# Optimization experiments

Hardware: AMD Instinct MI355X
Metric: run time of the kernel (lower is better)

The kernel has to match this reference:

```python
import jax, jax.numpy as jnp
import numpy as np

B, T, N, D, H = 16, 16, 184, 128, 8
HD = D // H  # 16
EMB = 10


def _forward(dim, query, key, value, Wq, bq, Wk, bk, Wv, bv, Wm, bm, Wo, bo, ne1, ne2):
    B0 = query.shape[0]
    D0 = Wq.shape[0]
    HD0 = Wm.shape[0]
    H0 = D0 // HD0
    q = query @ Wq.T + bq
    k = key @ Wk.T + bk
    v = value @ Wv.T + bv

    def split_heads(x):  # [B, A, C, D] -> [H*B, A, C, HD], head-major (torch split+cat)
        x = x.reshape(x.shape[:-1] + (H0, HD0))
        x = jnp.moveaxis(x, -2, 0)  # [H, B, A, C, HD]
        return x.reshape((H0 * B0,) + x.shape[2:])

    q, k, v = split_heads(q), split_heads(k), split_heads(v)
    # attention over the last spatial axis: scores [H*B, T, N, N]
    attn = jnp.matmul(q, jnp.swapaxes(k, -1, -2)) / jnp.sqrt(jnp.asarray(HD0, q.dtype))
    attn_row = jax.nn.softmax(attn, axis=-1)
    attn_col = jax.nn.softmax(attn, axis=-2)
    o1 = jnp.matmul(attn_row, v)
    o2 = jnp.matmul(jnp.swapaxes(attn_col, -1, -2), v)
    adp = ne1 @ ne2  # [184, 184]
    adp_row = jax.nn.softmax(adp, axis=-1)
    adp_col = jax.nn.softmax(adp, axis=0)
    if dim == 2:
        o3 = jnp.einsum('ik,btkf->btif', adp_row, v)
        o4 = jnp.einsum('ik,btkf->btif', adp_col.T, v)
        out = jnp.concatenate([o1, o2, o3, o4], axis=-1)  # [H*B, T, N, 4*HD]
        out = out @ Wm.T + bm  # [H*B, T, N, HD]
    else:  # dim == 1
        o3 = jnp.einsum('ik,bktf->bitf', adp_row, v)
        o4 = jnp.einsum('ik,bktf->bitf', adp_col.T, v)
        cat = jnp.concatenate([o1, o2, o3, o4], axis=-1)
        filt = cat @ Wm.T + bm
        gate = jnp.tanh(cat[..., :HD0]) * jax.nn.sigmoid(cat[..., -HD0:])
        out = filt + gate
    # merge heads back: [H*B, ..., HD] -> [B, ..., H*HD]
    out = out.reshape((H0, B0) + out.shape[1:])
    out = jnp.moveaxis(out, 0, -2)
    out = out.reshape(out.shape[:-2] + (H0 * HD0,))
    return out @ Wo.T + bo


def setup_inputs() -> dict:
    rng = jax.random.key(0)
    ks = jax.random.split(rng, 16)
    n = lambda i, shape, s=1.0: jax.random.normal(ks[i], shape, dtype=jnp.float32) * s
    return {
        'query': n(0, (B, T, N, D)),
        'key': n(1, (B, T, N, D)),
        'value': n(2, (B, T, N, D)),
        'Wq': n(3, (D, D), 0.05), 'bq': n(4, (D,), 0.05),
        'Wk': n(5, (D, D), 0.05), 'bk': n(6, (D,), 0.05),
        'Wv': n(7, (D, D), 0.05), 'bv': n(8, (D,), 0.05),
        'Wm': n(9, (HD, 4 * HD), 0.05), 'bm': n(10, (HD,), 0.05),
        'Wo': n(11, (D, D), 0.05), 'bo': n(12, (D,), 0.05),
        'ne1': n(13, (N, EMB)),
        'ne2': n(14, (EMB, N)),
        'dim': 2,
    }


def reference(query, key, value, Wq, bq, Wk, bk, Wv, bv, Wm, bm, Wo, bo, ne1, ne2, dim):
    return _forward(dim, query, key, value, Wq, bq, Wk, bk, Wv, bv, Wm, bm, Wo, bo, ne1, ne2)
```

## Files before the change

kernel.cpp:

```cpp
#include <hip/hip_runtime.h>

typedef unsigned int u32;
typedef unsigned short u16;
typedef unsigned long long ull;

constexpr int kB = 16, kT = 16, kN = 184, kD = 128, kH = 8, kHD = 16;
constexpr int kBT = kB * kT;
constexpr int kRows = kBT * kN;
constexpr int kTile = kN * kHD;
#define KQSCALE 0.36067376022224085f

typedef __attribute__((ext_vector_type(8))) short bf16x8;
typedef __attribute__((ext_vector_type(4))) float f32x4;

union FragU {
  bf16x8 f;
  ull u[2];
  uint4 q;
  u16 h[8];
};

#define MFMA(a, b, c) __builtin_amdgcn_mfma_f32_16x16x32_bf16((a), (b), (c), 0, 0, 0)

__device__ __forceinline__ float bf2f(u16 v) {
  return __uint_as_float(((u32)v) << 16);
}
__device__ __forceinline__ u16 f2bf(float f) {
  u32 x = __float_as_uint(f);
  x += 0x7fffu + ((x >> 16) & 1u);
  return (u16)(x >> 16);
}
__device__ __forceinline__ u32 pack_bf2(float lo, float hi) {
  u32 a = __float_as_uint(lo); a += 0x7fffu + ((a >> 16) & 1u);
  u32 b = __float_as_uint(hi); b += 0x7fffu + ((b >> 16) & 1u);
  return __builtin_amdgcn_perm(b, a, 0x07060302);
}
__device__ __forceinline__ u32 pack_trunc(float lo, float hi) {
  return __builtin_amdgcn_perm(__float_as_uint(hi), __float_as_uint(lo), 0x07060302);
}
__device__ __forceinline__ u16 trunc_bf(float f) {
  return (u16)(__float_as_uint(f) >> 16);
}

__global__ __launch_bounds__(256) void proj_kernel(
    const float* __restrict__ qin, const float* __restrict__ kin, const float* __restrict__ vin,
    const float* __restrict__ Wq, const float* __restrict__ Wk, const float* __restrict__ Wv,
    const float* __restrict__ bq, const float* __restrict__ bk, const float* __restrict__ bv,
    u16* __restrict__ qo, u16* __restrict__ ko, u16* __restrict__ vo,
    const float* __restrict__ ne1, const float* __restrict__ ne2,
    u16* __restrict__ arr3, u16* __restrict__ arr4) {
  __shared__ float smem_f[17408];
  const int tid = threadIdx.x;

  if (blockIdx.y == 3) {
    if (blockIdx.x >= 12) return;
    float* const s1  = smem_f;
    float* const s2  = smem_f + 1840;
    float* const l1r = smem_f + 3680;
    float* const l2c = smem_f + 3864;

    for (int i = tid; i < kN * 10; i += 256) { s1[i] = ne1[i]; s2[i] = ne2[i]; }
    __syncthreads();

    if (tid < kN) {
      const int r = tid;
      float reg[10];
#pragma unroll
      for (int e = 0; e < 10; ++e) reg[e] = s1[r * 10 + e];
      float sum = 0.f;
      for (int c = 0; c < kN; ++c) {
        float d = 0.f;
#pragma unroll
        for (int e = 0; e < 10; ++e) d += reg[e] * s2[e * kN + c];
        sum += __expf(d);
      }
      l1r[r] = sum;

      const int c = tid;
      float regc[10];
#pragma unroll
      for (int e = 0; e < 10; ++e) regc[e] = s2[e * kN + c];
      sum = 0.f;
      for (int r2 = 0; r2 < kN; ++r2) {
        float d = 0.f;
#pragma unroll
        for (int e = 0; e < 10; ++e) d += s1[r2 * 10 + e] * regc[e];
        sum += __expf(d);
      }
      l2c[c] = sum;
    }
    __syncthreads();

    for (int ee = blockIdx.x * 256 + tid; ee < 12 * 6 * 64; ee += 12 * 256) {
      const int i = ee / 384;
      const int rem = ee - i * 384;
      const int p = rem >> 6;
      const int lane = rem & 63;
      const int row = i * 16 + (lane & 15);
      const int cb = p * 32 + (lane >> 4) * 8;
      FragU fo3, fo4;
      const bool rok = row < kN;
      float inv1 = 0.f, inv2 = 0.f;
      float rreg[10], creg[10];
      if (rok) {
        inv1 = 1.f / l1r[row];
        inv2 = 1.f / l2c[row];
#pragma unroll
        for (int e = 0; e < 10; ++e) {
          rreg[e] = s1[row * 10 + e];
          creg[e] = s2[e * kN + row];
        }
      }
#pragma unroll
      for (int j = 0; j < 8; ++j) {
        const int col = cb + j;
        float v3 = 0.f, v4 = 0.f;
        if (rok && col < kN) {
          float d3 = 0.f, d4 = 0.f;
#pragma unroll
          for (int e = 0; e < 10; ++e) {
            d3 += rreg[e] * s2[e * kN + col];
            d4 += s1[col * 10 + e] * creg[e];
          }
          v3 = __expf(d3) * inv1;
          v4 = __expf(d4) * inv2;
        }
        fo3.h[j] = f2bf(v3);
        fo4.h[j] = f2bf(v4);
      }
      *(uint4*)(arr3 + (size_t)ee * 8) = fo3.q;
      *(uint4*)(arr4 + (size_t)ee * 8) = fo4.q;
    }
    return;
  }

  u16* const s_w = (u16*)smem_f;
  u16* const s_a = (u16*)smem_f + 128 * 136;

  const float* in; const float* Wf; const float* bias; u16* out; float scale;
  if (blockIdx.y == 0)      { in = qin; Wf = Wq; bias = bq; out = qo; scale = KQSCALE; }
  else if (blockIdx.y == 1) { in = kin; Wf = Wk; bias = bk; out = ko; scale = 1.f; }
  else                      { in = vin; Wf = Wv; bias = bv; out = vo; scale = 1.f; }

  const int r0 = blockIdx.x * 128;
  {
    for (int i = tid; i < 2048; i += 256) {
      const int row = i >> 4, c8 = (i & 15) * 8;
      const float4 w0 = *(const float4*)(Wf + row * 128 + c8);
      const float4 w1 = *(const float4*)(Wf + row * 128 + c8 + 4);
      *(uint4*)(s_w + row * 136 + c8) =
          make_uint4(pack_bf2(w0.x, w0.y), pack_bf2(w0.z, w0.w),
                     pack_bf2(w1.x, w1.y), pack_bf2(w1.z, w1.w));
    }
    const float* abase = in + (size_t)r0 * 128;
#pragma unroll
    for (int i = 0; i < 16; ++i) {
      const int idx = i * 1024 + tid * 4;
      const float4 v = *(const float4*)(abase + idx);
      const int row = idx >> 7, col = idx & 127;
      *(u32*)(s_a + row * 136 + col)     = pack_bf2(v.x, v.y);
      *(u32*)(s_a + row * 136 + col + 2) = pack_bf2(v.z, v.w);
    }
  }
  __syncthreads();

  const int w = tid >> 6, lane = tid & 63, quad = lane >> 4, m = lane & 15;

  f32x4 acc0[8], acc1[8];
  const f32x4 z4 = {0.f, 0.f, 0.f, 0.f};
#pragma unroll
  for (int ct = 0; ct < 8; ++ct) { acc0[ct] = z4; acc1[ct] = z4; }

  const u16* ap0 = s_a + (w * 16 + m) * 136 + quad * 8;
  const u16* ap1 = ap0 + 64 * 136;

#pragma unroll
  for (int kp = 0; kp < 4; ++kp) {
    FragU a0; a0.q = *(const uint4*)(ap0 + kp * 32);
    FragU a1; a1.q = *(const uint4*)(ap1 + kp * 32);
#pragma unroll
    for (int ct = 0; ct < 8; ++ct) {
      FragU bfr; bfr.q = *(const uint4*)(s_w + (ct * 16 + m) * 136 + kp * 32 + quad * 8);
      acc0[ct] = MFMA(a0.f, bfr.f, acc0[ct]);
      acc1[ct] = MFMA(a1.f, bfr.f, acc1[ct]);
    }
  }

  float bc[8];
#pragma unroll
  for (int ct = 0; ct < 8; ++ct) bc[ct] = bias[ct * 16 + m];

#pragma unroll
  for (int half = 0; half < 2; ++half) {
    const f32x4* acc = half ? acc1 : acc0;
    const int rbase = r0 + (w + half * 4) * 16 + quad * 4;
#pragma unroll
    for (int rr = 0; rr < 4; ++rr) {
      const int r = rbase + rr;
      const int bt = r / kN;
      const int n = r - bt * kN;
      u16* op = out + ((size_t)bt * kN + n) * 16 + m;
#pragma unroll
      for (int ct = 0; ct < 8; ++ct)
        op[(size_t)ct * kBT * kN * 16] = f2bf((acc[ct][rr] + bc[ct]) * scale);
    }
  }
}

__global__ __launch_bounds__(256, 2) void attn_kernel(
    const u16* qg, const u16* __restrict__ kg, const u16* __restrict__ vg,
    const u16* __restrict__ arr3, const u16* __restrict__ arr4,
    const float* __restrict__ Wm, const float* __restrict__ bm,
    u16* mg) {
  __shared__ u16 pool[39424];
  u16* const s_E   = pool;
  u16* const s_ET0 = pool + 13824;
  u16* const s_ET1 = pool + 26624;
  u16* const s_vT  = s_ET1;
  u16* const s_cat = s_ET1;

  const int tid = threadIdx.x;
  const size_t base = (size_t)blockIdx.x * kTile;
  const int w = tid >> 6, lane = tid & 63;
  const int quad = lane >> 4, m = lane & 15;

  for (int idx = tid; idx < 3072; idx += 256) {
    const int t = idx >> 4, ch = idx & 15;
    s_vT[ch * 200 + t] = (t < kN) ? vg[base + idx] : (u16)0;
  }

  bf16x8 kfr[12];
#pragma unroll
  for (int t12 = 0; t12 < 12; ++t12) {
    FragU fk; fk.u[0] = 0; fk.u[1] = 0;
    const int tok = t12 * 16 + m;
    if (quad < 2 && tok < kN)
      fk.q = *(const uint4*)(kg + base + tok * 16 + quad * 8);
    kfr[t12] = fk.f;
  }
  bf16x8 qB[3];
#pragma unroll
  for (int ti = 0; ti < 3; ++ti) {
    FragU fq; fq.u[0] = 0; fq.u[1] = 0;
    const int tok = (w + ti * 4) * 16 + m;
    if (quad < 2 && tok < kN)
      fq.q = *(const uint4*)(qg + base + tok * 16 + quad * 8);
    qB[ti] = fq.f;
  }

  bf16x8 wmb[2];
#pragma unroll
  for (int kt = 0; kt < 2; ++kt) {
    FragU f;
#pragma unroll
    for (int j = 0; j < 8; ++j) {
      const int kdl = quad * 8 + j;
      const int orig = (kt * 2 + (kdl & 1)) * 16 + (kdl >> 1);
      f.h[j] = f2bf(Wm[m * 64 + orig]);
    }
    wmb[kt] = f.f;
  }
  const float4 bm4 = *(const float4*)(bm + quad * 4);

  __syncthreads();

  bf16x8 vb[6];
#pragma unroll
  for (int p = 0; p < 6; ++p) {
    FragU f;
    f.q = *(const uint4*)(s_vT + m * 200 + p * 32 + quad * 8);
    vb[p] = f.f;
  }
  FragU onesU; onesU.u[0] = 0x3F803F803F803F80ULL; onesU.u[1] = onesU.u[0];
  const bf16x8 ones = onesU.f;
  const f32x4 zero4 = {0.f, 0.f, 0.f, 0.f};

  f32x4 o1[3], l1[3], o3[3], o4[3], o2[3], l2[3];
#pragma unroll
  for (int ti = 0; ti < 3; ++ti) {
    o1[ti] = zero4; l1[ti] = zero4; o3[ti] = zero4;
    o4[ti] = zero4; o2[ti] = zero4; l2[ti] = zero4;
  }

#define S_PHASE(CC, ETB)                                                      \
  do {                                                                        \
    _Pragma("unroll") for (int ti = 0; ti < 3; ++ti) {                        \
      const int qt = w + ti * 4;                                              \
      const int qrow = qt * 16 + m;                                           \
      _Pragma("unroll") for (int ktl = 0; ktl < 4; ++ktl) {                   \
        f32x4 sv = MFMA(kfr[(CC) * 4 + ktl], qB[ti], zero4);                  \
        const float e0 = exp2f(sv[0]), e1 = exp2f(sv[1]);                     \
        const float e2 = exp2f(sv[2]), e3 = exp2f(sv[3]);                     \
        uint2 ev;                                                             \
        ev.x = pack_trunc(e0, e1);                                            \
        ev.y = pack_trunc(e2, e3);                                            \
        *(uint2*)(s_E + qrow * 72 + ktl * 16 + quad * 4) = ev;                \
        u16* etp = (ETB) + (ktl * 16 + quad * 4) * 200 + qrow;                \
        etp[0]   = trunc_bf(e0);                                              \
        etp[200] = trunc_bf(e1);                                              \
        etp[400] = trunc_bf(e2);                                              \
        etp[600] = trunc_bf(e3);                                              \
      }                                                                       \
    }                                                                         \
  } while (0)

#define LOAD_ARR(CC)                                                          \
  _Pragma("unroll") for (int ti = 0; ti < 3; ++ti) {                          \
    const int qt = w + ti * 4;                                                \
    _Pragma("unroll") for (int pl = 0; pl < 2; ++pl) {                        \
      const int pg = (CC) * 2 + pl;                                           \
      a3f[ti * 2 + pl].q = *(const uint4*)(arr3 + (size_t)((qt * 6 + pg) * 64 + lane) * 8); \
      a4f[ti * 2 + pl].q = *(const uint4*)(arr4 + (size_t)((qt * 6 + pg) * 64 + lane) * 8); \
    }                                                                         \
  }

#define ROW_PHASE(CC)                                                         \
  _Pragma("unroll") for (int ti = 0; ti < 3; ++ti) {                          \
    const int qt = w + ti * 4;                                                \
    const u16* erp = s_E + (qt * 16 + m) * 72 + quad * 8;                     \
    _Pragma("unroll") for (int pl = 0; pl < 2; ++pl) {                        \
      const int pg = (CC) * 2 + pl;                                           \
      FragU pa; pa.q = *(const uint4*)(erp + pl * 32);                        \
      o1[ti] = MFMA(pa.f, vb[pg], o1[ti]);                                    \
      l1[ti] = MFMA(pa.f, ones, l1[ti]);                                      \
      o3[ti] = MFMA(a3f[ti * 2 + pl].f, vb[pg], o3[ti]);                      \
      o4[ti] = MFMA(a4f[ti * 2 + pl].f, vb[pg], o4[ti]);                      \
    }                                                                         \
  }

#define COL_PHASE(CC, ETB)                                                    \
  {                                                                           \
    const u16* etr = (ETB) + (w * 16 + m) * 200 + quad * 8;                   \
    _Pragma("unroll") for (int pg = 0; pg < 6; ++pg) {                        \
      FragU pT; pT.q = *(const uint4*)(etr + pg * 32);                        \
      o2[CC] = MFMA(pT.f, vb[pg], o2[CC]);                                    \
      l2[CC] = MFMA(pT.f, ones, l2[CC]);                                      \
    }                                                                         \
  }

  S_PHASE(0, s_ET0);
  __syncthreads();
  {
    FragU a3f[6], a4f[6];
    LOAD_ARR(0);
    COL_PHASE(0, s_ET0);
    ROW_PHASE(0);
    S_PHASE(1, s_ET1);
  }
  __syncthreads();
  {
    FragU a3f[6], a4f[6];
    LOAD_ARR(1);
    COL_PHASE(1, s_ET1);
    ROW_PHASE(1);
    S_PHASE(2, s_ET0);
  }
  __syncthreads();
  {
    FragU a3f[6], a4f[6];
    LOAD_ARR(2);
    COL_PHASE(2, s_ET0);
    ROW_PHASE(2);
  }

#undef S_PHASE
#undef LOAD_ARR
#undef ROW_PHASE
#undef COL_PHASE

  u16* cw = s_cat + w * 1152;
#pragma unroll
  for (int ti = 0; ti < 3; ++ti) {
    const int tt = w + ti * 4;
#pragma unroll
    for (int r = 0; r < 4; ++r) {
      const int token = quad * 4 + r;
      const float n1 = o1[ti][r] * __builtin_amdgcn_rcpf(l1[ti][r] - 8.0f);
      const float n2 = o2[ti][r] * __builtin_amdgcn_rcpf(l2[ti][r] - 8.0f);
      *(u32*)(cw + token * 72 + 2 * m)      = pack_bf2(n1, n2);
      *(u32*)(cw + token * 72 + 32 + 2 * m) = pack_bf2(o3[ti][r], o4[ti][r]);
    }
    f32x4 macc = {bm4.x, bm4.y, bm4.z, bm4.w};
#pragma unroll
    for (int kt = 0; kt < 2; ++kt) {
      FragU ca; ca.q = *(const uint4*)(cw + m * 72 + kt * 32 + quad * 8);
      macc = MFMA(wmb[kt], ca.f, macc);
    }
    if (tt * 16 + m < kN) {
      *(uint2*)(mg + base + (tt * 16 + m) * 16 + quad * 4) =
          make_uint2(pack_bf2(macc[0], macc[1]), pack_bf2(macc[2], macc[3]));
    }
  }
}

__global__ __launch_bounds__(256) void out_kernel(
    const u16* __restrict__ mg, const float* __restrict__ Wo,
    const float* __restrict__ bo, float* __restrict__ outg) {
  __shared__ u16 s_w[128 * 136];
  const int tid = threadIdx.x;
  {
    for (int i = tid; i < 2048; i += 256) {
      const int row = i >> 4, c8 = (i & 15) * 8;
      const float4 w0 = *(const float4*)(Wo + row * 128 + c8);
      const float4 w1 = *(const float4*)(Wo + row * 128 + c8 + 4);
      *(uint4*)(s_w + row * 136 + c8) =
          make_uint4(pack_bf2(w0.x, w0.y), pack_bf2(w0.z, w0.w),
                     pack_bf2(w1.x, w1.y), pack_bf2(w1.z, w1.w));
    }
  }
  __syncthreads();

  const int w = tid >> 6, lane = tid & 63, quad = lane >> 4, m = lane & 15;
  const int r0 = blockIdx.x * 128;

  f32x4 acc0[8], acc1[8];
  const f32x4 z4 = {0.f, 0.f, 0.f, 0.f};
#pragma unroll
  for (int ct = 0; ct < 8; ++ct) { acc0[ct] = z4; acc1[ct] = z4; }

  const int hh = quad >> 1, hd8 = (quad & 1) * 8;
  const int ra = r0 + w * 16 + m;
  const int bt0 = ra / kN, n0 = ra - bt0 * kN;
  const int rb = ra + 64;
  const int bt1 = rb / kN, n1 = rb - bt1 * kN;
  const u16* mp0 = mg + ((size_t)(hh * kBT + bt0) * kN + n0) * 16 + hd8;
  const u16* mp1 = mg + ((size_t)(hh * kBT + bt1) * kN + n1) * 16 + hd8;
  const size_t hstep = (size_t)2 * kBT * kN * 16;

#pragma unroll
  for (int kp = 0; kp < 4; ++kp) {
    FragU a0; a0.q = *(const uint4*)(mp0 + kp * hstep);
    FragU a1; a1.q = *(const uint4*)(mp1 + kp * hstep);
#pragma unroll
    for (int ct = 0; ct < 8; ++ct) {
      FragU bfr; bfr.q = *(const uint4*)(s_w + (ct * 16 + m) * 136 + kp * 32 + quad * 8);
      acc0[ct] = MFMA(a0.f, bfr.f, acc0[ct]);
      acc1[ct] = MFMA(a1.f, bfr.f, acc1[ct]);
    }
  }

  float bc[8];
#pragma unroll
  for (int ct = 0; ct < 8; ++ct) bc[ct] = bo[ct * 16 + m];

#pragma unroll
  for (int half = 0; half < 2; ++half) {
    const f32x4* acc = half ? acc1 : acc0;
    const int rbase = r0 + (w + half * 4) * 16 + quad * 4;
#pragma unroll
    for (int rr = 0; rr < 4; ++rr) {
      float* op = outg + (size_t)(rbase + rr) * 128 + m;
#pragma unroll
      for (int ct = 0; ct < 8; ++ct)
        op[ct * 16] = acc[ct][rr] + bc[ct];
    }
  }
}

extern "C" void kernel_launch(void* const* d_in, const int* in_sizes, int n_in,
                              void* d_out, int out_size, void* d_ws, size_t ws_size,
                              hipStream_t stream) {
  const float* query = (const float*)d_in[0];
  const float* key   = (const float*)d_in[1];
  const float* value = (const float*)d_in[2];
  const float* Wq = (const float*)d_in[3];
  const float* bq = (const float*)d_in[4];
  const float* Wk = (const float*)d_in[5];
  const float* bk = (const float*)d_in[6];
  const float* Wv = (const float*)d_in[7];
  const float* bv = (const float*)d_in[8];
  const float* Wm = (const float*)d_in[9];
  const float* bm = (const float*)d_in[10];
  const float* Wo = (const float*)d_in[11];
  const float* bo = (const float*)d_in[12];
  const float* ne1 = (const float*)d_in[13];
  const float* ne2 = (const float*)d_in[14];

  const size_t tensor_bytes = (size_t)kH * kB * kT * kN * kHD * 2;
  const size_t frag_bytes = (size_t)12 * 6 * 64 * 8 * 2;
  char* ws = (char*)d_ws;
  u16* qs   = (u16*)(ws);
  u16* ks   = (u16*)(ws + tensor_bytes);
  u16* vs   = (u16*)(ws + 2 * tensor_bytes);
  u16* arr3 = (u16*)(ws + 3 * tensor_bytes);
  u16* arr4 = (u16*)(ws + 3 * tensor_bytes + frag_bytes);

  proj_kernel<<<dim3(kRows / 128, 4), 256, 0, stream>>>(
      query, key, value, Wq, Wk, Wv, bq, bk, bv, qs, ks, vs,
      ne1, ne2, arr3, arr4);
  attn_kernel<<<kH * kB * kT, 256, 0, stream>>>(qs, ks, vs, arr3, arr4, Wm, bm, qs);
  out_kernel<<<kRows / 128, 256, 0, stream>>>(qs, Wo, bo, (float*)d_out);
}
```

Baseline: 230.0 us.

## Fuse QKV projection into attention kernel, split adaptive-adjacency into own kernel

The separate QKV projection kernel is removed. Each attention block now projects its own head's q, k and v slices from the fp32 inputs with MFMA and keeps them in shared memory, so the bf16 q/k/v tensors no longer round-trip through global memory. The adjacency softmax work moves into a small standalone kernel. The cost is that each input row is now read once per head (8 times) instead of once, and each block does extra MFMA work before the attention phase, traded against the saved global writes and reads.

Result: slower. 292.8 us (+27.3%).

```diff
diff --git a/kernel.cpp b/kernel.cpp
--- a/kernel.cpp
+++ b/kernel.cpp
@@ -42,192 +42,183 @@
   return (u16)(__float_as_uint(f) >> 16);
 }
 
-__global__ __launch_bounds__(256) void proj_kernel(
+__global__ __launch_bounds__(256) void adp_kernel(
+    const float* __restrict__ ne1, const float* __restrict__ ne2,
+    u16* __restrict__ arr3, u16* __restrict__ arr4) {
+  __shared__ float s1[kN * 10];
+  __shared__ float s2[10 * kN];
+  __shared__ float l1r[kN];
+  __shared__ float l2c[kN];
+  const int tid = threadIdx.x;
+  for (int i = tid; i < kN * 10; i += 256) { s1[i] = ne1[i]; s2[i] = ne2[i]; }
+  __syncthreads();
+
+  if (tid < kN) {
+    const int r = tid;
+    float reg[10];
+#pragma unroll
+    for (int e = 0; e < 10; ++e) reg[e] = s1[r * 10 + e];
+    float sum = 0.f;
+    for (int c = 0; c < kN; ++c) {
+      float d = 0.f;
+#pragma unroll
+      for (int e = 0; e < 10; ++e) d += reg[e] * s2[e * kN + c];
+      sum += __expf(d);
+    }
+    l1r[r] = sum;
+
+    const int c = tid;
+    float regc[10];
+#pragma unroll
+    for (int e = 0; e < 10; ++e) regc[e] = s2[e * kN + c];
+    sum = 0.f;
+    for (int r2 = 0; r2 < kN; ++r2) {
+      float d = 0.f;
+#pragma unroll
+      for (int e = 0; e < 10; ++e) d += s1[r2 * 10 + e] * regc[e];
+      sum += __expf(d);
+    }
+    l2c[c] = sum;
+  }
+  __syncthreads();
+
+  for (int ee = blockIdx.x * 256 + tid; ee < 12 * 6 * 64; ee += 12 * 256) {
+    const int i = ee / 384;
+    const int rem = ee - i * 384;
+    const int p = rem >> 6;
+    const int lane = rem & 63;
+    const int row = i * 16 + (lane & 15);
+    const int cb = p * 32 + (lane >> 4) * 8;
+    FragU fo3, fo4;
+    const bool rok = row < kN;
+    float inv1 = 0.f, inv2 = 0.f;
+    float rreg[10], creg[10];
+    if (rok) {
+      inv1 = 1.f / l1r[row];
+      inv2 = 1.f / l2c[row];
+#pragma unroll
+      for (int e = 0; e < 10; ++e) {
+        rreg[e] = s1[row * 10 + e];
+        creg[e] = s2[e * kN + row];
+      }
+    }
+#pragma unroll
+    for (int j = 0; j < 8; ++j) {
+      const int col = cb + j;
+      float v3 = 0.f, v4 = 0.f;
+      if (rok && col < kN) {
+        float d3 = 0.f, d4 = 0.f;
+#pragma unroll
+        for (int e = 0; e < 10; ++e) {
+          d3 += rreg[e] * s2[e * kN + col];
+          d4 += s1[col * 10 + e] * creg[e];
+        }
+        v3 = __expf(d3) * inv1;
+        v4 = __expf(d4) * inv2;
+      }
+      fo3.h[j] = f2bf(v3);
+      fo4.h[j] = f2bf(v4);
+    }
+    *(uint4*)(arr3 + (size_t)ee * 8) = fo3.q;
+    *(uint4*)(arr4 + (size_t)ee * 8) = fo4.q;
+  }
+}
+
+__global__ __launch_bounds__(256, 2) void attn_kernel(
     const float* __restrict__ qin, const float* __restrict__ kin, const float* __restrict__ vin,
     const float* __restrict__ Wq, const float* __restrict__ Wk, const float* __restrict__ Wv,
     const float* __restrict__ bq, const float* __restrict__ bk, const float* __restrict__ bv,
-    u16* __restrict__ qo, u16* __restrict__ ko, u16* __restrict__ vo,
-    const float* __restrict__ ne1, const float* __restrict__ ne2,
-    u16* __restrict__ arr3, u16* __restrict__ arr4) {
-  __shared__ float smem_f[17408];
-  const int tid = threadIdx.x;
-
-  if (blockIdx.y == 3) {
-    if (blockIdx.x >= 12) return;
-    float* const s1  = smem_f;
-    float* const s2  = smem_f + 1840;
-    float* const l1r = smem_f + 3680;
-    float* const l2c = smem_f + 3864;
-
-    for (int i = tid; i < kN * 10; i += 256) { s1[i] = ne1[i]; s2[i] = ne2[i]; }
-    __syncthreads();
-
-    if (tid < kN) {
-      const int r = tid;
-      float reg[10];
-#pragma unroll
-      for (int e = 0; e < 10; ++e) reg[e] = s1[r * 10 + e];
-      float sum = 0.f;
-      for (int c = 0; c < kN; ++c) {
-        float d = 0.f;
-#pragma unroll
-        for (int e = 0; e < 10; ++e) d += reg[e] * s2[e * kN + c];
-        sum += __expf(d);
-      }
-      l1r[r] = sum;
-
-      const int c = tid;
-      float regc[10];
-#pragma unroll
-      for (int e = 0; e < 10; ++e) regc[e] = s2[e * kN + c];
-      sum = 0.f;
-      for (int r2 = 0; r2 < kN; ++r2) {
-        float d = 0.f;
-#pragma unroll
-        for (int e = 0; e < 10; ++e) d += s1[r2 * 10 + e] * regc[e];
-        sum += __expf(d);
-      }
-      l2c[c] = sum;
-    }
-    __syncthreads();
-
-    for (int ee = blockIdx.x * 256 + tid; ee < 12 * 6 * 64; ee += 12 * 256) {
-      const int i = ee / 384;
-      const int rem = ee - i * 384;
-      const int p = rem >> 6;
-      const int lane = rem & 63;
-      const int row = i * 16 + (lane & 15);
-      const int cb = p * 32 + (lane >> 4) * 8;
-      FragU fo3, fo4;
-      const bool rok = row < kN;
-      float inv1 = 0.f, inv2 = 0.f;
-      float rreg[10], creg[10];
-      if (rok) {
-        inv1 = 1.f / l1r[row];
-        inv2 = 1.f / l2c[row];
-#pragma unroll
-        for (int e = 0; e < 10; ++e) {
-          rreg[e] = s1[row * 10 + e];
-          creg[e] = s2[e * kN + row];
-        }
-      }
-#pragma unroll
-      for (int j = 0; j < 8; ++j) {
-        const int col = cb + j;
-        float v3 = 0.f, v4 = 0.f;
-        if (rok && col < kN) {
-          float d3 = 0.f, d4 = 0.f;
-#pragma unroll
-          for (int e = 0; e < 10; ++e) {
-            d3 += rreg[e] * s2[e * kN + col];
-            d4 += s1[col * 10 + e] * creg[e];
-          }
-          v3 = __expf(d3) * inv1;
-          v4 = __expf(d4) * inv2;
-        }
-        fo3.h[j] = f2bf(v3);
-        fo4.h[j] = f2bf(v4);
-      }
-      *(uint4*)(arr3 + (size_t)ee * 8) = fo3.q;
-      *(uint4*)(arr4 + (size_t)ee * 8) = fo4.q;
-    }
-    return;
-  }
-
-  u16* const s_w = (u16*)smem_f;
-  u16* const s_a = (u16*)smem_f + 128 * 136;
-
-  const float* in; const float* Wf; const float* bias; u16* out; float scale;
-  if (blockIdx.y == 0)      { in = qin; Wf = Wq; bias = bq; out = qo; scale = KQSCALE; }
-  else if (blockIdx.y == 1) { in = kin; Wf = Wk; bias = bk; out = ko; scale = 1.f; }
-  else                      { in = vin; Wf = Wv; bias = bv; out = vo; scale = 1.f; }
-
-  const int r0 = blockIdx.x * 128;
-  {
-    for (int i = tid; i < 2048; i += 256) {
-      const int row = i >> 4, c8 = (i & 15) * 8;
-      const float4 w0 = *(const float4*)(Wf + row * 128 + c8);
-      const float4 w1 = *(const float4*)(Wf + row * 128 + c8 + 4);
-      *(uint4*)(s_w + row * 136 + c8) =
-          make_uint4(pack_bf2(w0.x, w0.y), pack_bf2(w0.z, w0.w),
-                     pack_bf2(w1.x, w1.y), pack_bf2(w1.z, w1.w));
-    }
-    const float* abase = in + (size_t)r0 * 128;
-#pragma unroll
-    for (int i = 0; i < 16; ++i) {
-      const int idx = i * 1024 + tid * 4;
-      const float4 v = *(const float4*)(abase + idx);
-      const int row = idx >> 7, col = idx & 127;
-      *(u32*)(s_a + row * 136 + col)     = pack_bf2(v.x, v.y);
-      *(u32*)(s_a + row * 136 + col + 2) = pack_bf2(v.z, v.w);
-    }
-  }
-  __syncthreads();
-
-  const int w = tid >> 6, lane = tid & 63, quad = lane >> 4, m = lane & 15;
-
-  f32x4 acc0[8], acc1[8];
-  const f32x4 z4 = {0.f, 0.f, 0.f, 0.f};
-#pragma unroll
-  for (int ct = 0; ct < 8; ++ct) { acc0[ct] = z4; acc1[ct] = z4; }
-
-  const u16* ap0 = s_a + (w * 16 + m) * 136 + quad * 8;
-  const u16* ap1 = ap0 + 64 * 136;
-
-#pragma unroll
-  for (int kp = 0; kp < 4; ++kp) {
-    FragU a0; a0.q = *(const uint4*)(ap0 + kp * 32);
-    FragU a1; a1.q = *(const uint4*)(ap1 + kp * 32);
-#pragma unroll
-    for (int ct = 0; ct < 8; ++ct) {
-      FragU bfr; bfr.q = *(const uint4*)(s_w + (ct * 16 + m) * 136 + kp * 32 + quad * 8);
-      acc0[ct] = MFMA(a0.f, bfr.f, acc0[ct]);
-      acc1[ct] = MFMA(a1.f, bfr.f, acc1[ct]);
-    }
-  }
-
-  float bc[8];
-#pragma unroll
-  for (int ct = 0; ct < 8; ++ct) bc[ct] = bias[ct * 16 + m];
-
-#pragma unroll
-  for (int half = 0; half < 2; ++half) {
-    const f32x4* acc = half ? acc1 : acc0;
-    const int rbase = r0 + (w + half * 4) * 16 + quad * 4;
-#pragma unroll
-    for (int rr = 0; rr < 4; ++rr) {
-      const int r = rbase + rr;
-      const int bt = r / kN;
-      const int n = r - bt * kN;
-      u16* op = out + ((size_t)bt * kN + n) * 16 + m;
-#pragma unroll
-      for (int ct = 0; ct < 8; ++ct)
-        op[(size_t)ct * kBT * kN * 16] = f2bf((acc[ct][rr] + bc[ct]) * scale);
-    }
-  }
-}
-
-__global__ __launch_bounds__(256, 2) void attn_kernel(
-    const u16* qg, const u16* __restrict__ kg, const u16* __restrict__ vg,
     const u16* __restrict__ arr3, const u16* __restrict__ arr4,
     const float* __restrict__ Wm, const float* __restrict__ bm,
-    u16* mg) {
+    u16* __restrict__ mg) {
   __shared__ u16 pool[39424];
   u16* const s_E   = pool;
   u16* const s_ET0 = pool + 13824;
   u16* const s_ET1 = pool + 26624;
-  u16* const s_vT  = s_ET1;
+  u16* const s_q   = pool + 13824;
+  u16* const s_k   = pool + 18432;
+  u16* const s_vT  = pool + 23040;
   u16* const s_cat = s_ET1;
 
   const int tid = threadIdx.x;
-  const size_t base = (size_t)blockIdx.x * kTile;
+  const int h  = blockIdx.x & 7;
+  const int bt = blockIdx.x >> 3;
+  const size_t base = (size_t)(h * kBT + bt) * kTile;
   const int w = tid >> 6, lane = tid & 63;
   const int quad = lane >> 4, m = lane & 15;
-
-  for (int idx = tid; idx < 3072; idx += 256) {
-    const int t = idx >> 4, ch = idx & 15;
-    s_vT[ch * 200 + t] = (t < kN) ? vg[base + idx] : (u16)0;
-  }
+  const f32x4 zero4 = {0.f, 0.f, 0.f, 0.f};
+
+#pragma unroll
+  for (int u = 0; u < 3; ++u) {
+    const float* in  = (u == 0) ? qin : (u == 1) ? kin : vin;
+    const float* Wt  = (u == 0) ? Wq  : (u == 1) ? Wk  : Wv;
+    const float* bs  = (u == 0) ? bq  : (u == 1) ? bk  : bv;
+    bf16x8 wf[4];
+#pragma unroll
+    for (int kp = 0; kp < 4; ++kp) {
+      const float* wp = Wt + (size_t)(h * 16 + m) * 128 + kp * 32 + quad * 8;
+      const float4 wa = *(const float4*)wp;
+      const float4 wb2 = *(const float4*)(wp + 4);
+      FragU f;
+      f.q = make_uint4(pack_bf2(wa.x, wa.y), pack_bf2(wa.z, wa.w),
+                       pack_bf2(wb2.x, wb2.y), pack_bf2(wb2.z, wb2.w));
+      wf[kp] = f.f;
+    }
+    const float bias = bs[h * 16 + m];
+#pragma unroll
+    for (int ti = 0; ti < 3; ++ti) {
+      const int n0 = (w + ti * 4) * 16;
+      f32x4 acc = zero4;
+#pragma unroll
+      for (int kp = 0; kp < 4; ++kp) {
+        FragU a; a.u[0] = 0; a.u[1] = 0;
+        const int row = n0 + m;
+        if (row < kN) {
+          const float* ap = in + ((size_t)bt * kN + row) * 128 + kp * 32 + quad * 8;
+          const float4 xa = *(const float4*)ap;
+          const float4 xb = *(const float4*)(ap + 4);
+          a.q = make_uint4(pack_bf2(xa.x, xa.y), pack_bf2(xa.z, xa.w),
+                           pack_bf2(xb.x, xb.y), pack_bf2(xb.z, xb.w));
+        }
+        acc = MFMA(a.f, wf[kp], acc);
+      }
+      if (u == 0) {
+#pragma unroll
+        for (int r = 0; r < 4; ++r)
+          s_q[(n0 + quad * 4 + r) * 24 + m] = f2bf((acc[r] + bias) * KQSCALE);
+      } else if (u == 1) {
+#pragma unroll
+        for (int r = 0; r < 4; ++r)
+          s_k[(n0 + quad * 4 + r) * 24 + m] = f2bf(acc[r] + bias);
+      } else {
+        const int tb = n0 + quad * 4;
+        const float v0 = (tb + 0 < kN) ? acc[0] + bias : 0.f;
+        const float v1 = (tb + 1 < kN) ? acc[1] + bias : 0.f;
+        const float v2 = (tb + 2 < kN) ? acc[2] + bias : 0.f;
+        const float v3 = (tb + 3 < kN) ? acc[3] + bias : 0.f;
+        uint2 pv;
+        pv.x = pack_bf2(v0, v1);
+        pv.y = pack_bf2(v2, v3);
+        *(uint2*)(s_vT + m * 200 + tb) = pv;
+      }
+    }
+  }
+
+  bf16x8 wmb[2];
+#pragma unroll
+  for (int kt = 0; kt < 2; ++kt) {
+    FragU f;
+#pragma unroll
+    for (int j = 0; j < 8; ++j) {
+      const int kdl = quad * 8 + j;
+      const int orig = (kt * 2 + (kdl & 1)) * 16 + (kdl >> 1);
+      f.h[j] = f2bf(Wm[m * 64 + orig]);
+    }
+    wmb[kt] = f.f;
+  }
+  const float4 bm4 = *(const float4*)(bm + quad * 4);
+
+  __syncthreads();
 
   bf16x8 kfr[12];
 #pragma unroll
@@ -235,7 +226,7 @@
     FragU fk; fk.u[0] = 0; fk.u[1] = 0;
     const int tok = t12 * 16 + m;
     if (quad < 2 && tok < kN)
-      fk.q = *(const uint4*)(kg + base + tok * 16 + quad * 8);
+      fk.q = *(const uint4*)(s_k + tok * 24 + quad * 8);
     kfr[t12] = fk.f;
   }
   bf16x8 qB[3];
@@ -244,26 +235,9 @@
     FragU fq; fq.u[0] = 0; fq.u[1] = 0;
     const int tok = (w + ti * 4) * 16 + m;
     if (quad < 2 && tok < kN)
-      fq.q = *(const uint4*)(qg + base + tok * 16 + quad * 8);
+      fq.q = *(const uint4*)(s_q + tok * 24 + quad * 8);
     qB[ti] = fq.f;
   }
-
-  bf16x8 wmb[2];
-#pragma unroll
-  for (int kt = 0; kt < 2; ++kt) {
-    FragU f;
-#pragma unroll
-    for (int j = 0; j < 8; ++j) {
-      const int kdl = quad * 8 + j;
-      const int orig = (kt * 2 + (kdl & 1)) * 16 + (kdl >> 1);
-      f.h[j] = f2bf(Wm[m * 64 + orig]);
-    }
-    wmb[kt] = f.f;
-  }
-  const float4 bm4 = *(const float4*)(bm + quad * 4);
-
-  __syncthreads();
-
   bf16x8 vb[6];
 #pragma unroll
   for (int p = 0; p < 6; ++p) {
@@ -271,9 +245,11 @@
     f.q = *(const uint4*)(s_vT + m * 200 + p * 32 + quad * 8);
     vb[p] = f.f;
   }
+
+  __syncthreads();
+
   FragU onesU; onesU.u[0] = 0x3F803F803F803F80ULL; onesU.u[1] = onesU.u[0];
   const bf16x8 ones = onesU.f;
-  const f32x4 zero4 = {0.f, 0.f, 0.f, 0.f};
 
   f32x4 o1[3], l1[3], o3[3], o4[3], o2[3], l2[3];
 #pragma unroll
@@ -479,15 +455,12 @@
   const size_t tensor_bytes = (size_t)kH * kB * kT * kN * kHD * 2;
   const size_t frag_bytes = (size_t)12 * 6 * 64 * 8 * 2;
   char* ws = (char*)d_ws;
-  u16* qs   = (u16*)(ws);
-  u16* ks   = (u16*)(ws + tensor_bytes);
-  u16* vs   = (u16*)(ws + 2 * tensor_bytes);
-  u16* arr3 = (u16*)(ws + 3 * tensor_bytes);
-  u16* arr4 = (u16*)(ws + 3 * tensor_bytes + frag_bytes);
-
-  proj_kernel<<<dim3(kRows / 128, 4), 256, 0, stream>>>(
-      query, key, value, Wq, Wk, Wv, bq, bk, bv, qs, ks, vs,
-      ne1, ne2, arr3, arr4);
-  attn_kernel<<<kH * kB * kT, 256, 0, stream>>>(qs, ks, vs, arr3, arr4, Wm, bm, qs);
-  out_kernel<<<kRows / 128, 256, 0, stream>>>(qs, Wo, bo, (float*)d_out);
-}
+  u16* mgs  = (u16*)(ws);
+  u16* arr3 = (u16*)(ws + tensor_bytes);
+  u16* arr4 = (u16*)(ws + tensor_bytes + frag_bytes);
+
+  adp_kernel<<<12, 256, 0, stream>>>(ne1, ne2, arr3, arr4);
+  attn_kernel<<<kH * kB * kT, 256, 0, stream>>>(
+      query, key, value, Wq, Wk, Wv, bq, bk, bv, arr3, arr4, Wm, bm, mgs);
+  out_kernel<<<kRows / 128, 256, 0, stream>>>(mgs, Wo, bo, (float*)d_out);
+}
```
